# Optimization experiments

Measured on AMD Instinct MI355X. Metric: run time of the kernel, lower is better.

The kernel has to match this reference:

```python
import math
import jax, jax.numpy as jnp
import numpy as np

V, D, H, NL, C, F, L, B = 32000, 1024, 16, 6, 10, 4096, 512, 16
DK = D // H
EPS = 1e-5


def _make_pe(max_len, d_model):
    pos = np.arange(max_len, dtype=np.float32)[:, None]
    div = np.exp(np.arange(0, d_model, 2, dtype=np.float32) * (-math.log(10000.0) / d_model))
    pe = np.zeros((max_len, d_model), np.float32)
    pe[:, 0::2] = np.sin(pos * div)
    pe[:, 1::2] = np.cos(pos * div)
    return jnp.asarray(pe)


def setup_inputs() -> dict:
    key = jax.random.key(0)
    ks = jax.random.split(key, 12)
    s = 0.02
    n = lambda k, shape: jax.random.normal(k, shape, jnp.float32) * s
    return {
        "input_ids": jax.random.randint(ks[0], (B, L), 0, V, dtype=jnp.int64),
        "emb": n(ks[1], (V, D)),
        "pe": _make_pe(L, D),
        "wq": n(ks[2], (D, D)), "bq": jnp.zeros((D,), jnp.float32),
        "wk": n(ks[3], (D, D)), "bk": jnp.zeros((D,), jnp.float32),
        "wv": n(ks[4], (D, D)), "bv": jnp.zeros((D,), jnp.float32),
        "wo": n(ks[5], (D, D)), "bo": jnp.zeros((D,), jnp.float32),
        "w1": n(ks[6], (D, F)), "b1": jnp.zeros((F,), jnp.float32),
        "w2": n(ks[7], (F, D)), "b2": jnp.zeros((D,), jnp.float32),
        "g1": jnp.ones((D,), jnp.float32), "be1": jnp.zeros((D,), jnp.float32),
        "g2": jnp.ones((D,), jnp.float32), "be2": jnp.zeros((D,), jnp.float32),
        "wf": n(ks[8], (D, C)), "bf": jnp.zeros((C,), jnp.float32),
    }


def _layernorm(x, g, b):
    m = jnp.mean(x, axis=-1, keepdims=True)
    v = jnp.mean(jnp.square(x - m), axis=-1, keepdims=True)
    return (x - m) * jax.lax.rsqrt(v + EPS) * g + b


def _forward(input_ids, emb, pe, wq, bq, wk, bk, wv, bv, wo, bo,
             w1, b1, w2, b2, g1, be1, g2, be2, wf, bf):
    x = emb[input_ids] * jnp.sqrt(jnp.float32(D))  # [B,L,D]
    x = x + pe[None, :x.shape[1], :]
    scale = 1.0 / math.sqrt(DK)
    for _ in range(NL):  # shared weights across all layers (faithful to source)
        bsz, sl, _ = x.shape
        q = (x @ wq + bq).reshape(bsz, sl, H, DK).transpose(0, 2, 1, 3)
        k = (x @ wk + bk).reshape(bsz, sl, H, DK).transpose(0, 2, 1, 3)
        v = (x @ wv + bv).reshape(bsz, sl, H, DK).transpose(0, 2, 1, 3)
        scores = jnp.einsum('bhqd,bhkd->bhqk', q, k) * scale
        p = jax.nn.softmax(scores, axis=-1)
        o = jnp.einsum('bhqk,bhkd->bhqd', p, v)
        o = o.transpose(0, 2, 1, 3).reshape(bsz, sl, D)
        attn_out = o @ wo + bo            # [B,L,D]
        src2 = attn_out[0]                # faithful to `self.self_attn(...)[0]` -> [L,D], broadcast over batch
        x = _layernorm(x + src2, g1, be1)
        ff = (x @ w1 + b1) @ w2 + b2      # NOTE: no activation in the source FFN
        x = _layernorm(x + ff, g2, be2)
    pooled = jnp.mean(x, axis=1)          # [B,D]
    return pooled @ wf + bf               # [B,C]


def reference(input_ids, emb, pe, wq, bq, wk, bk, wv, bv, wo, bo,
              w1, b1, w2, b2, g1, be1, g2, be2, wf, bf):
    return _forward(input_ids, emb, pe, wq, bq, wk, bk, wv, bv, wo, bo,
                    w1, b1, w2, b2, g1, be1, g2, be2, wf, bf)
```

## Files before the change

### kernel.cpp

```cpp
#include <hip/hip_runtime.h>

typedef unsigned short u16;
typedef unsigned int u32;
typedef __bf16 bf16x8 __attribute__((ext_vector_type(8)));
typedef float f32x4 __attribute__((ext_vector_type(4)));

#define LN_EPS 1e-5f
#define L2E 1.44269504f

__device__ __forceinline__ u16 f2bf(float f) {
    u32 u = __float_as_uint(f);
    u += 0x7fffu + ((u >> 16) & 1u);
    return (u16)(u >> 16);
}
__device__ __forceinline__ float bf2f(u32 v) {
    return __uint_as_float(v << 16);
}
__device__ __forceinline__ void unp8(uint4 u, float* v) {
    v[0] = bf2f(u.x & 0xffff); v[1] = bf2f(u.x >> 16);
    v[2] = bf2f(u.y & 0xffff); v[3] = bf2f(u.y >> 16);
    v[4] = bf2f(u.z & 0xffff); v[5] = bf2f(u.z >> 16);
    v[6] = bf2f(u.w & 0xffff); v[7] = bf2f(u.w >> 16);
}
__device__ __forceinline__ u32 pk2(float a, float b) {
    return (u32)f2bf(a) | ((u32)f2bf(b) << 16);
}

#define ASYNC_CP16(g, l)                                                      \
    __builtin_amdgcn_global_load_lds(                                         \
        (const __attribute__((address_space(1))) u32*)(g),                    \
        (__attribute__((address_space(3))) u32*)(l), 16, 0, 0)

__global__ __launch_bounds__(256) void k_prep(
    const float* __restrict__ wq, const float* __restrict__ wk,
    const float* __restrict__ wv, const float* __restrict__ wo,
    const float* __restrict__ w1, const float* __restrict__ w2,
    const float* __restrict__ bq, const float* __restrict__ bk,
    const float* __restrict__ bv, float* __restrict__ qkvb,
    u16* __restrict__ wqkvT, u16* __restrict__ woT,
    u16* __restrict__ w1b, u16* __restrict__ w2T)
{
    int b = blockIdx.x;
    if (b >= 12288) {
        int i = (b - 12288) * 256 + threadIdx.x;
        qkvb[i] = (i < 1024) ? bq[i] : (i < 2048 ? bk[i - 1024] : bv[i - 2048]);
        return;
    }
    if (b >= 4096 && b < 8192) {
        int i = (b - 4096) * 1024 + threadIdx.x * 4;
        float4 v = *(const float4*)&w1[i];
        ushort4 o;
        o.x = f2bf(v.x); o.y = f2bf(v.y); o.z = f2bf(v.z); o.w = f2bf(v.w);
        *(ushort4*)&w1b[i] = o;
        return;
    }
    const float* in; u16* out; int C; long ldo; int gx; int l;
    if (b < 4096) {
        int j = b >> 10; l = b & 1023;
        in = (j == 0) ? wq : (j == 1) ? wk : (j == 2) ? wv : wo;
        out = (j == 3) ? woT : wqkvT + (long)j * 1024 * 1024;
        C = 1024; ldo = 1024; gx = 32;
    } else {
        l = b - 8192; in = w2; out = w2T; C = 1024; ldo = 4096; gx = 32;
    }
    int bx = l % gx, by = l / gx;
    __shared__ float tile[32][33];
    int c0 = bx * 32, r0 = by * 32;
    int tx = threadIdx.x & 31, ty = threadIdx.x >> 5;
#pragma unroll
    for (int i = 0; i < 4; i++)
        tile[ty + 8 * i][tx] = in[(long)(r0 + ty + 8 * i) * C + c0 + tx];
    __syncthreads();
#pragma unroll
    for (int i = 0; i < 4; i++)
        out[(long)(c0 + ty + 8 * i) * ldo + r0 + tx] = f2bf(tile[tx][ty + 8 * i]);
}

__global__ __launch_bounds__(256) void k_bias12a(
    const float* __restrict__ b1, const float* __restrict__ w2,
    float* __restrict__ partial)
{
    int eb = blockIdx.x & 7;
    int fc = blockIdx.x >> 3;
    int t = threadIdx.x;
    int e = eb * 128 + (t & 127);
    int f0 = fc * 128 + (t >> 7) * 64;
    float s = 0.f;
    for (int f = f0; f < f0 + 64; f++)
        s += b1[f] * w2[(long)f * 1024 + e];
    __shared__ float sh[256];
    sh[t] = s;
    __syncthreads();
    if (t < 128) partial[(long)fc * 1024 + e] = sh[t] + sh[t + 128];
}

__global__ __launch_bounds__(128) void k_bias12b(
    const float* __restrict__ partial, const float* __restrict__ b2,
    float* __restrict__ b12)
{
    int e = blockIdx.x * 128 + threadIdx.x;
    float s = b2[e];
#pragma unroll 8
    for (int fc = 0; fc < 32; fc++) s += partial[(long)fc * 1024 + e];
    b12[e] = s;
}

__global__ __launch_bounds__(256) void k_embed(
    const int* __restrict__ ids, const float* __restrict__ emb,
    const float* __restrict__ pe, u16* __restrict__ xb)
{
    int row = blockIdx.x;
    int l = row & 511;
    long id = (long)ids[row];
    const float* e = emb + id * 1024;
    const float* p = pe + (long)l * 1024;
    u16* xbo = xb + (long)row * 1024;
    int d0 = threadIdx.x * 4;
    float4 ev = *(const float4*)&e[d0];
    float4 pv = *(const float4*)&p[d0];
    ushort4 o;
    o.x = f2bf(ev.x * 32.0f + pv.x);
    o.y = f2bf(ev.y * 32.0f + pv.y);
    o.z = f2bf(ev.z * 32.0f + pv.z);
    o.w = f2bf(ev.w * 32.0f + pv.w);
    *(ushort4*)&xbo[d0] = o;
}

template <int TM, int TN, bool VT_EPI>
__global__ __launch_bounds__(256) void k_gemm_nt(
    const u16* __restrict__ A, long lda,
    const u16* __restrict__ B, long ldb,
    u16* __restrict__ Cm, long ldc,
    int M, int N, int K,
    const float* __restrict__ bias,
    u16* __restrict__ vTout)
{
    constexpr int FM = TM / 32;
    constexpr int FN = TN / 32;
    constexpr int CPA = TM / 64;
    constexpr int CPB = TN / 64;
    __shared__ u16 As[2 * TM * 32];
    __shared__ u16 Bs[2 * TN * 32];
    int m0 = blockIdx.y * TM, n0 = blockIdx.x * TN;
    int tid = threadIdx.x;
    int lane = tid & 63, wid = tid >> 6;
    int wr = wid >> 1, wc = wid & 1;
    int quad = lane >> 4, l16 = lane & 15;

    f32x4 acc[FM][FN];
#pragma unroll
    for (int i = 0; i < FM; i++)
#pragma unroll
        for (int j = 0; j < FN; j++) acc[i][j] = {0.f, 0.f, 0.f, 0.f};

    int seg = (lane & 3) * 8;
    const u16* pA[CPA]; u16* lA[2][CPA];
    const u16* pB[CPB]; u16* lB[2][CPB];
#pragma unroll
    for (int i = 0; i < CPA; i++) {
        int c = wid * CPA + i;
        int gm = min(m0 + c * 16 + (lane >> 2), M - 1);
        pA[i] = A + (long)gm * lda + seg;
        lA[0][i] = &As[c * 512];
        lA[1][i] = &As[TM * 32 + c * 512];
    }
#pragma unroll
    for (int i = 0; i < CPB; i++) {
        int c = wid * CPB + i;
        int gn = min(n0 + c * 16 + (lane >> 2), N - 1);
        pB[i] = B + (long)gn * ldb + seg;
        lB[0][i] = &Bs[c * 512];
        lB[1][i] = &Bs[TN * 32 + c * 512];
    }

    for (int kb = 0; kb < K; kb += 64) {
#pragma unroll
        for (int kh = 0; kh < 2; kh++) {
#pragma unroll
            for (int i = 0; i < CPA; i++) ASYNC_CP16(pA[i] + kb + kh * 32, lA[kh][i]);
#pragma unroll
            for (int i = 0; i < CPB; i++) ASYNC_CP16(pB[i] + kb + kh * 32, lB[kh][i]);
        }
        __syncthreads();
        bf16x8 af[2][FM], bg[2][FN];
#pragma unroll
        for (int kh = 0; kh < 2; kh++)
#pragma unroll
            for (int t = 0; t < FM; t++)
                af[kh][t] = *(const bf16x8*)&As[kh * TM * 32 + (wr * (TM / 2) + t * 16 + l16) * 32 + quad * 8];
#pragma unroll
        for (int kh = 0; kh < 2; kh++)
#pragma unroll
            for (int t = 0; t < FN; t++)
                bg[kh][t] = *(const bf16x8*)&Bs[kh * TN * 32 + (wc * (TN / 2) + t * 16 + l16) * 32 + quad * 8];
#pragma unroll
        for (int kh = 0; kh < 2; kh++)
#pragma unroll
            for (int i = 0; i < FM; i++)
#pragma unroll
                for (int j = 0; j < FN; j++)
                    acc[i][j] = __builtin_amdgcn_mfma_f32_16x16x32_bf16(af[kh][i], bg[kh][j], acc[i][j], 0, 0, 0);
        __syncthreads();
    }

#pragma unroll
    for (int i = 0; i < FM; i++) {
        int gm0 = m0 + wr * (TM / 2) + i * 16 + quad * 4;
#pragma unroll
        for (int j = 0; j < FN; j++) {
            int gn = n0 + wc * (TN / 2) + j * 16 + l16;
            if (gn >= N) continue;
            float bn = bias ? bias[gn] : 0.f;
            if (VT_EPI && gn >= 2048) {
                ushort4 o;
                o.x = f2bf(acc[i][j][0] + bn);
                o.y = f2bf(acc[i][j][1] + bn);
                o.z = f2bf(acc[i][j][2] + bn);
                o.w = f2bf(acc[i][j][3] + bn);
                *(ushort4*)&vTout[(long)(gn - 2048) * 512 + gm0] = o;
                continue;
            }
#pragma unroll
            for (int r = 0; r < 4; r++) {
                int gm = gm0 + r;
                if (gm >= M) continue;
                Cm[(long)gm * ldc + gn] = f2bf(acc[i][j][r] + bn);
            }
        }
    }
}

template <bool SPLITK>
__global__ __launch_bounds__(512, 2) void k_gemm8(
    const u16* __restrict__ A, long lda,
    const u16* __restrict__ B, long ldb,
    u16* __restrict__ Cm, long ldc,
    int K, const float* __restrict__ bias)
{
    constexpr int BM = 256, BN = 256;
    constexpr int MF = 8;
    constexpr int ASLOT = BM * 32;
    constexpr int BSLOT = BN * 32;
    __shared__ u16 As[4 * ASLOT];
    __shared__ u16 Bs[4 * BSLOT];

    int lin = blockIdx.y * gridDim.x + blockIdx.x;
    int cpx = (gridDim.x * gridDim.y) >> 3;
    int sw = (lin & 7) * cpx + (lin >> 3);
    int bx = sw % gridDim.x, by = sw / gridDim.x;

    const int m0 = by * BM, n0 = bx * BN;
    const long kbase = SPLITK ? (long)blockIdx.z * K : 0;
    const int tid = threadIdx.x;
    const int lane = tid & 63, wid = tid >> 6;
    const int wm = wid >> 2, wn = wid & 3;
    const int wrow = wm * 128, wcol = wn * 64;
    const int quad = lane >> 4, l16 = lane & 15;

    f32x4 acc[MF][4];
#pragma unroll
    for (int f = 0; f < MF; f++)
#pragma unroll
        for (int g = 0; g < 4; g++) acc[f][g] = {0.f, 0.f, 0.f, 0.f};

    const int srow = wid * 16 + (lane >> 2);
    const int skoff = (((lane & 3) ^ ((lane >> 3) & 3)) << 3);
    const u16* aSrc = A + (long)(m0 + srow) * lda + kbase + skoff;
    const u16* bSrc = B + (long)(n0 + srow) * ldb + kbase + skoff;

    int aoff[MF], boff[4];
#pragma unroll
    for (int f = 0; f < MF; f++) {
        int r = wrow + f * 16 + l16;
        aoff[f] = r * 32 + ((quad ^ ((r >> 1) & 3)) << 3);
    }
#pragma unroll
    for (int g = 0; g < 4; g++) {
        int r = wcol + g * 16 + l16;
        boff[g] = r * 32 + ((quad ^ ((r >> 1) & 3)) << 3);
    }

    auto stageA = [&](int j) {
        u16* d = &As[(j & 3) * ASLOT + wid * 512];
#pragma unroll
        for (int i = 0; i < 2; i++)
            ASYNC_CP16(aSrc + (long)i * 128 * lda + j * 32, d + i * 4096);
    };
    auto stageB = [&](int j) {
        u16* d = &Bs[(j & 3) * BSLOT + wid * 512];
#pragma unroll
        for (int i = 0; i < 2; i++)
            ASYNC_CP16(bSrc + (long)i * 128 * ldb + j * 32, d + i * 4096);
    };

    stageA(0); stageB(0); stageA(1); stageB(1); stageA(2); stageB(2);
    asm volatile("s_waitcnt vmcnt(4)" ::: "memory");
    __builtin_amdgcn_s_barrier();

    bf16x8 ra[2][MF], rb[2][4];
#pragma unroll
    for (int f = 0; f < MF; f++) ra[0][f] = *(const bf16x8*)&As[aoff[f]];
#pragma unroll
    for (int g = 0; g < 4; g++)  rb[0][g] = *(const bf16x8*)&Bs[boff[g]];

    const int NK = K >> 5;
    for (int j0 = 0; j0 < NK - 2; j0 += 2) {
#pragma unroll
        for (int u = 0; u < 2; u++) {
            const int j = j0 + u;
            const u16* Abn = &As[((j + 1) & 3) * ASLOT];
            const u16* Bbn = &Bs[((j + 1) & 3) * BSLOT];
#pragma unroll
            for (int f = 0; f < MF; f++) ra[u ^ 1][f] = *(const bf16x8*)&Abn[aoff[f]];
#pragma unroll
            for (int g = 0; g < 4; g++)  rb[u ^ 1][g] = *(const bf16x8*)&Bbn[boff[g]];
            if (j + 3 < NK) { stageA(j + 3); stageB(j + 3); }
            __builtin_amdgcn_sched_barrier(0);
            asm volatile("s_waitcnt lgkmcnt(12)" ::: "memory");
            __builtin_amdgcn_sched_barrier(0);
            __builtin_amdgcn_s_setprio(1);
#pragma unroll
            for (int f = 0; f < MF; f++)
#pragma unroll
                for (int g = 0; g < 4; g++)
                    acc[f][g] = __builtin_amdgcn_mfma_f32_16x16x32_bf16(ra[u][f], rb[u][g], acc[f][g], 0, 0, 0);
            __builtin_amdgcn_s_setprio(0);
            if (j < NK - 3) asm volatile("s_waitcnt vmcnt(4)" ::: "memory");
            else            asm volatile("s_waitcnt vmcnt(0)" ::: "memory");
            __builtin_amdgcn_s_barrier();
        }
    }
    {
        const u16* Abn = &As[((NK - 1) & 3) * ASLOT];
        const u16* Bbn = &Bs[((NK - 1) & 3) * BSLOT];
#pragma unroll
        for (int f = 0; f < MF; f++) ra[1][f] = *(const bf16x8*)&Abn[aoff[f]];
#pragma unroll
        for (int g = 0; g < 4; g++)  rb[1][g] = *(const bf16x8*)&Bbn[boff[g]];
        __builtin_amdgcn_sched_barrier(0);
        asm volatile("s_waitcnt lgkmcnt(12)" ::: "memory");
        __builtin_amdgcn_sched_barrier(0);
        __builtin_amdgcn_s_setprio(1);
#pragma unroll
        for (int f = 0; f < MF; f++)
#pragma unroll
            for (int g = 0; g < 4; g++)
                acc[f][g] = __builtin_amdgcn_mfma_f32_16x16x32_bf16(ra[0][f], rb[0][g], acc[f][g], 0, 0, 0);
        __builtin_amdgcn_s_setprio(0);
    }
    {
        asm volatile("s_waitcnt lgkmcnt(0)" ::: "memory");
        __builtin_amdgcn_sched_barrier(0);
        __builtin_amdgcn_s_setprio(1);
#pragma unroll
        for (int f = 0; f < MF; f++)
#pragma unroll
            for (int g = 0; g < 4; g++)
                acc[f][g] = __builtin_amdgcn_mfma_f32_16x16x32_bf16(ra[1][f], rb[1][g], acc[f][g], 0, 0, 0);
        __builtin_amdgcn_s_setprio(0);
    }

    if (SPLITK) {
        float* Co = (float*)Cm + (long)blockIdx.z * (long)gridDim.y * BM * ldc;
        const bool zb = (blockIdx.z == 0);
#pragma unroll
        for (int f = 0; f < MF; f++) {
            int gm0 = m0 + wrow + f * 16 + quad * 4;
#pragma unroll
            for (int g = 0; g < 4; g++) {
                int gn = n0 + wcol + g * 16 + l16;
                float bn = zb ? bias[gn] : 0.f;
#pragma unroll
                for (int r = 0; r < 4; r++)
                    Co[(long)(gm0 + r) * ldc + gn] = acc[f][g][r] + bn;
            }
        }
    } else {
#pragma unroll
        for (int f = 0; f < MF; f++) {
            int gm0 = m0 + wrow + f * 16 + quad * 4;
#pragma unroll
            for (int g = 0; g < 4; g++) {
                int gn = n0 + wcol + g * 16 + l16;
                float bn = bias[gn];
#pragma unroll
                for (int r = 0; r < 4; r++)
                    Cm[(long)(gm0 + r) * ldc + gn] = f2bf(acc[f][g][r] + bn);
            }
        }
    }
}

__global__ __launch_bounds__(128) void k_attn(
    const u16* __restrict__ qkv, const u16* __restrict__ vT, u16* __restrict__ Ob)
{
    __shared__ u16 Ks[2][4096];
    __shared__ u16 Vs[2][4096];
    __shared__ u16 Pl[32 * 72];
    int qb = blockIdx.x, h = blockIdx.y;
    int tid = threadIdx.x;
    int w = tid >> 6, lane = tid & 63;
    int quad = lane >> 4, l16 = lane & 15;

    int qrow = qb * 32 + w * 16 + l16;
    bf16x8 aq[2];
#pragma unroll
    for (int c = 0; c < 2; c++)
        aq[c] = *(const bf16x8*)&qkv[(long)qrow * 3072 + h * 64 + c * 32 + quad * 8];

    f32x4 acc_o[4];
#pragma unroll
    for (int j = 0; j < 4; j++) acc_o[j] = {0.f, 0.f, 0.f, 0.f};
    float mrow[4], lrow[4];
#pragma unroll
    for (int r = 0; r < 4; r++) { mrow[r] = -1e30f; lrow[r] = 0.f; }

    {
        int kt = 0;
#pragma unroll
        for (int rr = 0; rr < 4; rr++) {
            int c = rr * 2 + w;
            int loc = (c & 3) * 16 + (lane >> 2);
            int off8 = ((c >> 2) << 5) + (lane & 3) * 8;
            ASYNC_CP16(&qkv[(long)(kt * 64 + loc) * 3072 + 1024 + h * 64 + off8], &Ks[0][c * 512]);
            ASYNC_CP16(&vT[(long)(h * 64 + loc) * 512 + kt * 64 + off8], &Vs[0][c * 512]);
        }
    }
    __syncthreads();

    for (int kt = 0; kt < 8; kt++) {
        int buf = kt & 1;
        if (kt < 7) {
            int nb = buf ^ 1, ktn = kt + 1;
#pragma unroll
            for (int rr = 0; rr < 4; rr++) {
                int c = rr * 2 + w;
                int loc = (c & 3) * 16 + (lane >> 2);
                int off8 = ((c >> 2) << 5) + (lane & 3) * 8;
                ASYNC_CP16(&qkv[(long)(ktn * 64 + loc) * 3072 + 1024 + h * 64 + off8], &Ks[nb][c * 512]);
                ASYNC_CP16(&vT[(long)(h * 64 + loc) * 512 + ktn * 64 + off8], &Vs[nb][c * 512]);
            }
        }
        f32x4 s[4];
#pragma unroll
        for (int ss = 0; ss < 4; ss++) {
            s[ss] = {0.f, 0.f, 0.f, 0.f};
#pragma unroll
            for (int c = 0; c < 2; c++) {
                bf16x8 bk = *(const bf16x8*)&Ks[buf][c * 2048 + (ss * 16 + l16) * 32 + quad * 8];
                s[ss] = __builtin_amdgcn_mfma_f32_16x16x32_bf16(aq[c], bk, s[ss], 0, 0, 0);
            }
        }
        float mt[4];
#pragma unroll
        for (int r = 0; r < 4; r++) {
#pragma unroll
            for (int ss = 0; ss < 4; ss++) s[ss][r] *= 0.125f;
            mt[r] = fmaxf(fmaxf(s[0][r], s[1][r]), fmaxf(s[2][r], s[3][r]));
        }
#pragma unroll
        for (int mask = 1; mask < 16; mask <<= 1)
#pragma unroll
            for (int r = 0; r < 4; r++) mt[r] = fmaxf(mt[r], __shfl_xor(mt[r], mask));
        float al[4], rsum[4];
#pragma unroll
        for (int r = 0; r < 4; r++) {
            float mn = fmaxf(mrow[r], mt[r]);
            al[r] = exp2f((mrow[r] - mn) * L2E);
            mrow[r] = mn;
            rsum[r] = 0.f;
#pragma unroll
            for (int ss = 0; ss < 4; ss++) {
                float p = exp2f((s[ss][r] - mn) * L2E);
                s[ss][r] = p;
                rsum[r] += p;
            }
        }
#pragma unroll
        for (int mask = 1; mask < 16; mask <<= 1)
#pragma unroll
            for (int r = 0; r < 4; r++) rsum[r] += __shfl_xor(rsum[r], mask);
#pragma unroll
        for (int r = 0; r < 4; r++) lrow[r] = lrow[r] * al[r] + rsum[r];
#pragma unroll
        for (int j = 0; j < 4; j++)
#pragma unroll
            for (int r = 0; r < 4; r++) acc_o[j][r] *= al[r];
#pragma unroll
        for (int ss = 0; ss < 4; ss++)
#pragma unroll
            for (int r = 0; r < 4; r++)
                Pl[(w * 16 + quad * 4 + r) * 72 + ss * 16 + l16] = f2bf(s[ss][r]);
#pragma unroll
        for (int kc = 0; kc < 2; kc++) {
            bf16x8 ap = *(const bf16x8*)&Pl[(w * 16 + l16) * 72 + kc * 32 + quad * 8];
#pragma unroll
            for (int j = 0; j < 4; j++) {
                bf16x8 bv = *(const bf16x8*)&Vs[buf][kc * 2048 + (j * 16 + l16) * 32 + quad * 8];
                acc_o[j] = __builtin_amdgcn_mfma_f32_16x16x32_bf16(ap, bv, acc_o[j], 0, 0, 0);
            }
        }
        __syncthreads();
    }

#pragma unroll
    for (int r = 0; r < 4; r++) {
        float inv = 1.0f / lrow[r];
        int gq = qb * 32 + w * 16 + quad * 4 + r;
#pragma unroll
        for (int j = 0; j < 4; j++)
            Ob[(long)gq * 1024 + h * 64 + j * 16 + l16] = f2bf(acc_o[j][r] * inv);
    }
}

__global__ __launch_bounds__(256) void k_add_ln(
    u16* __restrict__ xb, const u16* __restrict__ s, int sBroadcast,
    const float* __restrict__ g, const float* __restrict__ beta)
{
    int row = blockIdx.x * 4 + (threadIdx.x >> 6);
    int lane = threadIdx.x & 63;
    int srow = sBroadcast ? (row & 511) : row;
    u16* x = xb + (long)row * 1024;
    const u16* sp = s + (long)srow * 1024;
    int d0 = lane * 16;
    uint4 xa = *(const uint4*)&x[d0];
    uint4 xc = *(const uint4*)&x[d0 + 8];
    uint4 sa = *(const uint4*)&sp[d0];
    uint4 sc = *(const uint4*)&sp[d0 + 8];
    float v[16], t[8];
    unp8(xa, v); unp8(xc, v + 8);
    unp8(sa, t);
#pragma unroll
    for (int i = 0; i < 8; i++) v[i] += t[i];
    unp8(sc, t);
#pragma unroll
    for (int i = 0; i < 8; i++) v[8 + i] += t[i];
    float sum = 0.f, sq = 0.f;
#pragma unroll
    for (int i = 0; i < 16; i++) { sum += v[i]; sq += v[i] * v[i]; }
#pragma unroll
    for (int off = 32; off; off >>= 1) {
        sum += __shfl_xor(sum, off);
        sq += __shfl_xor(sq, off);
    }
    float mean = sum * (1.f / 1024.f);
    float var = sq * (1.f / 1024.f) - mean * mean;
    float rstd = rsqrtf(var + LN_EPS);
    float4 g0 = *(const float4*)&g[d0],      g1 = *(const float4*)&g[d0 + 4];
    float4 g2 = *(const float4*)&g[d0 + 8],  g3 = *(const float4*)&g[d0 + 12];
    float4 b0 = *(const float4*)&beta[d0],     b1 = *(const float4*)&beta[d0 + 4];
    float4 b2 = *(const float4*)&beta[d0 + 8], b3 = *(const float4*)&beta[d0 + 12];
    float gg[16] = {g0.x,g0.y,g0.z,g0.w, g1.x,g1.y,g1.z,g1.w, g2.x,g2.y,g2.z,g2.w, g3.x,g3.y,g3.z,g3.w};
    float bb[16] = {b0.x,b0.y,b0.z,b0.w, b1.x,b1.y,b1.z,b1.w, b2.x,b2.y,b2.z,b2.w, b3.x,b3.y,b3.z,b3.w};
    float y[16];
#pragma unroll
    for (int i = 0; i < 16; i++) y[i] = (v[i] - mean) * rstd * gg[i] + bb[i];
    uint4 oa, oc;
    oa.x = pk2(y[0], y[1]);  oa.y = pk2(y[2], y[3]);
    oa.z = pk2(y[4], y[5]);  oa.w = pk2(y[6], y[7]);
    oc.x = pk2(y[8], y[9]);  oc.y = pk2(y[10], y[11]);
    oc.z = pk2(y[12], y[13]); oc.w = pk2(y[14], y[15]);
    *(uint4*)&x[d0] = oa;
    *(uint4*)&x[d0 + 8] = oc;
}

__global__ __launch_bounds__(256) void k_add_ln2(
    u16* __restrict__ xb, const float* __restrict__ p0, const float* __restrict__ p1,
    const float* __restrict__ g, const float* __restrict__ beta)
{
    int row = blockIdx.x * 4 + (threadIdx.x >> 6);
    int lane = threadIdx.x & 63;
    u16* x = xb + (long)row * 1024;
    const float* a0 = p0 + (long)row * 1024;
    const float* a1 = p1 + (long)row * 1024;
    int d0 = lane * 16;
    uint4 xa = *(const uint4*)&x[d0];
    uint4 xc = *(const uint4*)&x[d0 + 8];
    float v[16];
    unp8(xa, v); unp8(xc, v + 8);
#pragma unroll
    for (int i = 0; i < 16; i += 4) {
        float4 q0 = *(const float4*)&a0[d0 + i];
        float4 q1 = *(const float4*)&a1[d0 + i];
        v[i]     += q0.x + q1.x;
        v[i + 1] += q0.y + q1.y;
        v[i + 2] += q0.z + q1.z;
        v[i + 3] += q0.w + q1.w;
    }
    float sum = 0.f, sq = 0.f;
#pragma unroll
    for (int i = 0; i < 16; i++) { sum += v[i]; sq += v[i] * v[i]; }
#pragma unroll
    for (int off = 32; off; off >>= 1) {
        sum += __shfl_xor(sum, off);
        sq += __shfl_xor(sq, off);
    }
    float mean = sum * (1.f / 1024.f);
    float var = sq * (1.f / 1024.f) - mean * mean;
    float rstd = rsqrtf(var + LN_EPS);
    float4 g0 = *(const float4*)&g[d0],      g1 = *(const float4*)&g[d0 + 4];
    float4 g2 = *(const float4*)&g[d0 + 8],  g3 = *(const float4*)&g[d0 + 12];
    float4 b0 = *(const float4*)&beta[d0],     b1 = *(const float4*)&beta[d0 + 4];
    float4 b2 = *(const float4*)&beta[d0 + 8], b3 = *(const float4*)&beta[d0 + 12];
    float gg[16] = {g0.x,g0.y,g0.z,g0.w, g1.x,g1.y,g1.z,g1.w, g2.x,g2.y,g2.z,g2.w, g3.x,g3.y,g3.z,g3.w};
    float bb[16] = {b0.x,b0.y,b0.z,b0.w, b1.x,b1.y,b1.z,b1.w, b2.x,b2.y,b2.z,b2.w, b3.x,b3.y,b3.z,b3.w};
    float y[16];
#pragma unroll
    for (int i = 0; i < 16; i++) y[i] = (v[i] - mean) * rstd * gg[i] + bb[i];
    uint4 oa, oc;
    oa.x = pk2(y[0], y[1]);  oa.y = pk2(y[2], y[3]);
    oa.z = pk2(y[4], y[5]);  oa.w = pk2(y[6], y[7]);
    oc.x = pk2(y[8], y[9]);  oc.y = pk2(y[10], y[11]);
    oc.z = pk2(y[12], y[13]); oc.w = pk2(y[14], y[15]);
    *(uint4*)&x[d0] = oa;
    *(uint4*)&x[d0 + 8] = oc;
}

__global__ __launch_bounds__(256) void k_pool_a(
    const u16* __restrict__ xb, float* __restrict__ pp)
{
    int b = blockIdx.x >> 3, ch = blockIdx.x & 7;
    int d0 = threadIdx.x * 4;
    const u16* x = xb + ((long)b * 512 + ch * 64) * 1024;
    float s0 = 0.f, s1 = 0.f, s2 = 0.f, s3 = 0.f;
    for (int l = 0; l < 64; l++) {
        ushort4 v = *(const ushort4*)&x[(long)l * 1024 + d0];
        s0 += bf2f(v.x); s1 += bf2f(v.y); s2 += bf2f(v.z); s3 += bf2f(v.w);
    }
    float* o = pp + ((long)b * 8 + ch) * 1024 + d0;
    o[0] = s0; o[1] = s1; o[2] = s2; o[3] = s3;
}

__global__ __launch_bounds__(256) void k_pool_b(
    const float* __restrict__ pp, const float* __restrict__ wf,
    const float* __restrict__ bfin, float* __restrict__ out)
{
    int b = blockIdx.x;
    int tid = threadIdx.x;
    __shared__ float pl[1024];
    int d0 = tid * 4;
    float s0 = 0.f, s1 = 0.f, s2 = 0.f, s3 = 0.f;
#pragma unroll
    for (int ch = 0; ch < 8; ch++) {
        float4 q = *(const float4*)&pp[((long)b * 8 + ch) * 1024 + d0];
        s0 += q.x; s1 += q.y; s2 += q.z; s3 += q.w;
    }
    pl[d0] = s0 * (1.f / 512.f);
    pl[d0 + 1] = s1 * (1.f / 512.f);
    pl[d0 + 2] = s2 * (1.f / 512.f);
    pl[d0 + 3] = s3 * (1.f / 512.f);
    __syncthreads();
    __shared__ float red[4];
    for (int c = 0; c < 10; c++) {
        float t = 0.f;
        for (int d = tid; d < 1024; d += 256) t += pl[d] * wf[(long)d * 10 + c];
        for (int off = 32; off; off >>= 1) t += __shfl_down(t, off);
        if ((tid & 63) == 0) red[tid >> 6] = t;
        __syncthreads();
        if (tid == 0) out[b * 10 + c] = red[0] + red[1] + red[2] + red[3] + bfin[c];
        __syncthreads();
    }
}

template <int TM, int TN, bool VT_EPI>
static void gemm(const u16* A, long lda, const u16* B, long ldb,
                 u16* C, long ldc,
                 int M, int N, int K, const float* bias,
                 hipStream_t st, u16* vTout = nullptr)
{
    dim3 g((N + TN - 1) / TN, (M + TM - 1) / TM);
    k_gemm_nt<TM, TN, VT_EPI><<<g, 256, 0, st>>>(A, lda, B, ldb, C, ldc, M, N, K, bias, vTout);
}

extern "C" void kernel_launch(void* const* d_in, const int* in_sizes, int n_in,
                              void* d_out, int out_size, void* d_ws, size_t ws_size,
                              hipStream_t stream)
{
    const int* ids   = (const int*)d_in[0];
    const float* emb = (const float*)d_in[1];
    const float* pe  = (const float*)d_in[2];
    const float* wq  = (const float*)d_in[3];
    const float* bq  = (const float*)d_in[4];
    const float* wk  = (const float*)d_in[5];
    const float* bk  = (const float*)d_in[6];
    const float* wv  = (const float*)d_in[7];
    const float* bv  = (const float*)d_in[8];
    const float* wo  = (const float*)d_in[9];
    const float* bo  = (const float*)d_in[10];
    const float* w1  = (const float*)d_in[11];
    const float* b1  = (const float*)d_in[12];
    const float* w2  = (const float*)d_in[13];
    const float* b2  = (const float*)d_in[14];
    const float* g1  = (const float*)d_in[15];
    const float* be1 = (const float*)d_in[16];
    const float* g2  = (const float*)d_in[17];
    const float* be2 = (const float*)d_in[18];
    const float* wf  = (const float*)d_in[19];
    const float* bfi = (const float*)d_in[20];
    float* out = (float*)d_out;

    char* base = (char*)d_ws;
    size_t off = 0;
    auto alloc = [&](size_t bytes) {
        char* p = base + off;
        off = (off + bytes + 255) & ~(size_t)255;
        return p;
    };
    u16*   xb    = (u16*)  alloc(16UL * 512 * 1024 * 2);
    u16*   wqkvT = (u16*)  alloc(3072UL * 1024 * 2);
    u16*   woT   = (u16*)  alloc(1024UL * 1024 * 2);
    u16*   w1b   = (u16*)  alloc(1024UL * 4096 * 2);
    u16*   w2T   = (u16*)  alloc(1024UL * 4096 * 2);
    u16*   W12T  = (u16*)  alloc(1024UL * 1024 * 2);
    float* b12f  = (float*)alloc(1024UL * 4);
    float* b12p  = (float*)alloc(32UL * 1024 * 4);
    float* qkvb  = (float*)alloc(3072UL * 4);
    u16*   qkv   = (u16*)  alloc(512UL * 3072 * 2);
    u16*   vT    = (u16*)  alloc(1024UL * 512 * 2);
    u16*   Ob    = (u16*)  alloc(512UL * 1024 * 2);
    u16*   src2  = (u16*)  alloc(512UL * 1024 * 2);
    float* ppool = (float*)alloc(16UL * 8 * 1024 * 4);
    float* ffp   = (float*)alloc(2UL * 8192 * 1024 * 4);

    k_prep<<<12300, 256, 0, stream>>>(wq, wk, wv, wo, w1, w2, bq, bk, bv, qkvb,
                                      wqkvT, woT, w1b, w2T);
    k_bias12a<<<256, 256, 0, stream>>>(b1, w2, b12p);
    k_bias12b<<<8, 128, 0, stream>>>(b12p, b2, b12f);
    k_embed<<<8192, 256, 0, stream>>>(ids, emb, pe, xb);
    gemm<64, 64, false>(w2T, 4096, w1b, 4096, W12T, 1024, 1024, 1024, 4096, nullptr, stream);

    for (int layer = 0; layer < 6; layer++) {
        gemm<64, 64, true>(xb, 1024, wqkvT, 1024, qkv, 3072, 512, 3072, 1024, qkvb, stream, vT);
        k_attn<<<dim3(16, 16), 128, 0, stream>>>(qkv, vT, Ob);
        gemm<64, 64, false>(Ob, 1024, woT, 1024, src2, 1024, 512, 1024, 1024, bo, stream);
        k_add_ln<<<2048, 256, 0, stream>>>(xb, src2, 1, g1, be1);
        k_gemm8<true><<<dim3(4, 32, 2), 512, 0, stream>>>(xb, 1024, W12T, 1024,
                                                          (u16*)ffp, 1024, 512, b12f);
        k_add_ln2<<<2048, 256, 0, stream>>>(xb, ffp, ffp + 8192UL * 1024, g2, be2);
    }

    k_pool_a<<<128, 256, 0, stream>>>(xb, ppool);
    k_pool_b<<<16, 256, 0, stream>>>(ppool, wf, bfi, out);
}
```

Before: 910.2 us.

## Fuse LN2 into next layer's LN1 and split-K the W12 precompute

The layer loop now fuses the FFN residual LayerNorm with the next layer's attention-residual LayerNorm into one kernel (k_ln2ln1). This removes a full read/write pass over the 16x512x1024 activations per layer. Because attention only uses batch row 0, a small k_ln_head kernel computes the LN2 output for the first 512 rows so the QKV GEMM can start before the full LN2 runs. The one-time W2·W1 product is moved to a split-K k_gemm8 launch (16 slices) followed by a reduction kernel, which adds an extra fp32 scratch pass over that product.

Measured after the change: 897.2 us. About the same (-1.4%).

```diff
diff --git a/kernel.cpp b/kernel.cpp
--- a/kernel.cpp
+++ b/kernel.cpp
@@ -103,6 +103,22 @@
 #pragma unroll 8
     for (int fc = 0; fc < 32; fc++) s += partial[(long)fc * 1024 + e];
     b12[e] = s;
+}
+
+__global__ __launch_bounds__(256) void k_w12red(
+    const float* __restrict__ p, u16* __restrict__ w12)
+{
+    int e = blockIdx.x;
+    int d0 = threadIdx.x * 4;
+    float4 s = {0.f, 0.f, 0.f, 0.f};
+#pragma unroll 4
+    for (int z = 0; z < 16; z++) {
+        float4 q = *(const float4*)&p[(long)z * 1024 * 1024 + (long)e * 1024 + d0];
+        s.x += q.x; s.y += q.y; s.z += q.z; s.w += q.w;
+    }
+    ushort4 o;
+    o.x = f2bf(s.x); o.y = f2bf(s.y); o.z = f2bf(s.z); o.w = f2bf(s.w);
+    *(ushort4*)&w12[(long)e * 1024 + d0] = o;
 }
 
 __global__ __launch_bounds__(256) void k_embed(
@@ -369,7 +385,7 @@
 #pragma unroll
             for (int g = 0; g < 4; g++) {
                 int gn = n0 + wcol + g * 16 + l16;
-                float bn = zb ? bias[gn] : 0.f;
+                float bn = (zb && bias) ? bias[gn] : 0.f;
 #pragma unroll
                 for (int r = 0; r < 4; r++)
                     Co[(long)(gm0 + r) * ldc + gn] = acc[f][g][r] + bn;
@@ -607,6 +623,145 @@
     float y[16];
 #pragma unroll
     for (int i = 0; i < 16; i++) y[i] = (v[i] - mean) * rstd * gg[i] + bb[i];
+    uint4 oa, oc;
+    oa.x = pk2(y[0], y[1]);  oa.y = pk2(y[2], y[3]);
+    oa.z = pk2(y[4], y[5]);  oa.w = pk2(y[6], y[7]);
+    oc.x = pk2(y[8], y[9]);  oc.y = pk2(y[10], y[11]);
+    oc.z = pk2(y[12], y[13]); oc.w = pk2(y[14], y[15]);
+    *(uint4*)&x[d0] = oa;
+    *(uint4*)&x[d0 + 8] = oc;
+}
+
+__global__ __launch_bounds__(256) void k_ln_head(
+    const u16* __restrict__ xb, const float* __restrict__ p0, const float* __restrict__ p1,
+    const float* __restrict__ g, const float* __restrict__ beta, u16* __restrict__ xhead)
+{
+    int row = blockIdx.x * 4 + (threadIdx.x >> 6);
+    int lane = threadIdx.x & 63;
+    const u16* x = xb + (long)row * 1024;
+    const float* a0 = p0 + (long)row * 1024;
+    const float* a1 = p1 + (long)row * 1024;
+    int d0 = lane * 16;
+    uint4 xa = *(const uint4*)&x[d0];
+    uint4 xc = *(const uint4*)&x[d0 + 8];
+    float v[16];
+    unp8(xa, v); unp8(xc, v + 8);
+#pragma unroll
+    for (int i = 0; i < 16; i += 4) {
+        float4 q0 = *(const float4*)&a0[d0 + i];
+        float4 q1 = *(const float4*)&a1[d0 + i];
+        v[i]     += q0.x + q1.x;
+        v[i + 1] += q0.y + q1.y;
+        v[i + 2] += q0.z + q1.z;
+        v[i + 3] += q0.w + q1.w;
+    }
+    float sum = 0.f, sq = 0.f;
+#pragma unroll
+    for (int i = 0; i < 16; i++) { sum += v[i]; sq += v[i] * v[i]; }
+#pragma unroll
+    for (int off = 32; off; off >>= 1) {
+        sum += __shfl_xor(sum, off);
+        sq += __shfl_xor(sq, off);
+    }
+    float mean = sum * (1.f / 1024.f);
+    float var = sq * (1.f / 1024.f) - mean * mean;
+    float rstd = rsqrtf(var + LN_EPS);
+    float y[16];
+#pragma unroll
+    for (int i = 0; i < 16; i += 4) {
+        float4 gv = *(const float4*)&g[d0 + i];
+        float4 bv = *(const float4*)&beta[d0 + i];
+        y[i]     = (v[i]     - mean) * rstd * gv.x + bv.x;
+        y[i + 1] = (v[i + 1] - mean) * rstd * gv.y + bv.y;
+        y[i + 2] = (v[i + 2] - mean) * rstd * gv.z + bv.z;
+        y[i + 3] = (v[i + 3] - mean) * rstd * gv.w + bv.w;
+    }
+    uint4 oa, oc;
+    oa.x = pk2(y[0], y[1]);  oa.y = pk2(y[2], y[3]);
+    oa.z = pk2(y[4], y[5]);  oa.w = pk2(y[6], y[7]);
+    oc.x = pk2(y[8], y[9]);  oc.y = pk2(y[10], y[11]);
+    oc.z = pk2(y[12], y[13]); oc.w = pk2(y[14], y[15]);
+    u16* o = xhead + (long)row * 1024;
+    *(uint4*)&o[d0] = oa;
+    *(uint4*)&o[d0 + 8] = oc;
+}
+
+__global__ __launch_bounds__(256) void k_ln2ln1(
+    u16* __restrict__ xb, const float* __restrict__ p0, const float* __restrict__ p1,
+    const u16* __restrict__ s2,
+    const float* __restrict__ g2, const float* __restrict__ be2,
+    const float* __restrict__ g1, const float* __restrict__ be1)
+{
+    int row = blockIdx.x * 4 + (threadIdx.x >> 6);
+    int lane = threadIdx.x & 63;
+    u16* x = xb + (long)row * 1024;
+    const float* a0 = p0 + (long)row * 1024;
+    const float* a1 = p1 + (long)row * 1024;
+    const u16* sp = s2 + (long)(row & 511) * 1024;
+    int d0 = lane * 16;
+    uint4 xa = *(const uint4*)&x[d0];
+    uint4 xc = *(const uint4*)&x[d0 + 8];
+    float v[16];
+    unp8(xa, v); unp8(xc, v + 8);
+#pragma unroll
+    for (int i = 0; i < 16; i += 4) {
+        float4 q0 = *(const float4*)&a0[d0 + i];
+        float4 q1 = *(const float4*)&a1[d0 + i];
+        v[i]     += q0.x + q1.x;
+        v[i + 1] += q0.y + q1.y;
+        v[i + 2] += q0.z + q1.z;
+        v[i + 3] += q0.w + q1.w;
+    }
+    float sum = 0.f, sq = 0.f;
+#pragma unroll
+    for (int i = 0; i < 16; i++) { sum += v[i]; sq += v[i] * v[i]; }
+#pragma unroll
+    for (int off = 32; off; off >>= 1) {
+        sum += __shfl_xor(sum, off);
+        sq += __shfl_xor(sq, off);
+    }
+    float mean = sum * (1.f / 1024.f);
+    float var = sq * (1.f / 1024.f) - mean * mean;
+    float rstd = rsqrtf(var + LN_EPS);
+#pragma unroll
+    for (int i = 0; i < 16; i += 4) {
+        float4 gv = *(const float4*)&g2[d0 + i];
+        float4 bv = *(const float4*)&be2[d0 + i];
+        v[i]     = (v[i]     - mean) * rstd * gv.x + bv.x;
+        v[i + 1] = (v[i + 1] - mean) * rstd * gv.y + bv.y;
+        v[i + 2] = (v[i + 2] - mean) * rstd * gv.z + bv.z;
+        v[i + 3] = (v[i + 3] - mean) * rstd * gv.w + bv.w;
+    }
+    uint4 sa = *(const uint4*)&sp[d0];
+    uint4 sc = *(const uint4*)&sp[d0 + 8];
+    float t[8];
+    unp8(sa, t);
+#pragma unroll
+    for (int i = 0; i < 8; i++) v[i] += t[i];
+    unp8(sc, t);
+#pragma unroll
+    for (int i = 0; i < 8; i++) v[8 + i] += t[i];
+    sum = 0.f; sq = 0.f;
+#pragma unroll
+    for (int i = 0; i < 16; i++) { sum += v[i]; sq += v[i] * v[i]; }
+#pragma unroll
+    for (int off = 32; off; off >>= 1) {
+        sum += __shfl_xor(sum, off);
+        sq += __shfl_xor(sq, off);
+    }
+    mean = sum * (1.f / 1024.f);
+    var = sq * (1.f / 1024.f) - mean * mean;
+    rstd = rsqrtf(var + LN_EPS);
+    float y[16];
+#pragma unroll
+    for (int i = 0; i < 16; i += 4) {
+        float4 gv = *(const float4*)&g1[d0 + i];
+        float4 bv = *(const float4*)&be1[d0 + i];
+        y[i]     = (v[i]     - mean) * rstd * gv.x + bv.x;
+        y[i + 1] = (v[i + 1] - mean) * rstd * gv.y + bv.y;
+        y[i + 2] = (v[i + 2] - mean) * rstd * gv.z + bv.z;
+        y[i + 3] = (v[i + 3] - mean) * rstd * gv.w + bv.w;
+    }
     uint4 oa, oc;
     oa.x = pk2(y[0], y[1]);  oa.y = pk2(y[2], y[3]);
     oa.z = pk2(y[4], y[5]);  oa.w = pk2(y[6], y[7]);
@@ -719,6 +874,7 @@
     u16*   vT    = (u16*)  alloc(1024UL * 512 * 2);
     u16*   Ob    = (u16*)  alloc(512UL * 1024 * 2);
     u16*   src2  = (u16*)  alloc(512UL * 1024 * 2);
+    u16*   xhead = (u16*)  alloc(512UL * 1024 * 2);
     float* ppool = (float*)alloc(16UL * 8 * 1024 * 4);
     float* ffp   = (float*)alloc(2UL * 8192 * 1024 * 4);
 
@@ -727,18 +883,29 @@
     k_bias12a<<<256, 256, 0, stream>>>(b1, w2, b12p);
     k_bias12b<<<8, 128, 0, stream>>>(b12p, b2, b12f);
     k_embed<<<8192, 256, 0, stream>>>(ids, emb, pe, xb);
-    gemm<64, 64, false>(w2T, 4096, w1b, 4096, W12T, 1024, 1024, 1024, 4096, nullptr, stream);
+    k_gemm8<true><<<dim3(4, 4, 16), 512, 0, stream>>>(w2T, 4096, w1b, 4096,
+                                                      (u16*)ffp, 1024, 256, nullptr);
+    k_w12red<<<1024, 256, 0, stream>>>(ffp, W12T);
 
     for (int layer = 0; layer < 6; layer++) {
-        gemm<64, 64, true>(xb, 1024, wqkvT, 1024, qkv, 3072, 512, 3072, 1024, qkvb, stream, vT);
+        const u16* qsrc = xb;
+        if (layer > 0) {
+            k_ln_head<<<128, 256, 0, stream>>>(xb, ffp, ffp + 8192UL * 1024, g2, be2, xhead);
+            qsrc = xhead;
+        }
+        gemm<64, 64, true>(qsrc, 1024, wqkvT, 1024, qkv, 3072, 512, 3072, 1024, qkvb, stream, vT);
         k_attn<<<dim3(16, 16), 128, 0, stream>>>(qkv, vT, Ob);
         gemm<64, 64, false>(Ob, 1024, woT, 1024, src2, 1024, 512, 1024, 1024, bo, stream);
-        k_add_ln<<<2048, 256, 0, stream>>>(xb, src2, 1, g1, be1);
+        if (layer == 0)
+            k_add_ln<<<2048, 256, 0, stream>>>(xb, src2, 1, g1, be1);
+        else
+            k_ln2ln1<<<2048, 256, 0, stream>>>(xb, ffp, ffp + 8192UL * 1024, src2,
+                                               g2, be2, g1, be1);
         k_gemm8<true><<<dim3(4, 32, 2), 512, 0, stream>>>(xb, 1024, W12T, 1024,
                                                           (u16*)ffp, 1024, 512, b12f);
-        k_add_ln2<<<2048, 256, 0, stream>>>(xb, ffp, ffp + 8192UL * 1024, g2, be2);
-    }
-
+    }
+
+    k_add_ln2<<<2048, 256, 0, stream>>>(xb, ffp, ffp + 8192UL * 1024, g2, be2);
     k_pool_a<<<128, 256, 0, stream>>>(xb, ppool);
     k_pool_b<<<16, 256, 0, stream>>>(ppool, wf, bfi, out);
 }
```
